# Kernel optimization log

Measured on AMD Instinct MI355X. Metric: run time of the kernel, lower is better.

## Reference

```python
import jax, jax.numpy as jnp
import numpy as np

N = 20000      # num_atoms
C = 64         # num_features (channels)
I = 16         # num_irreps = (l_max+1)^2, l_max=3
K2, K1, K0 = 120, 8, 4  # CG basis sizes per correlation order


def setup_inputs() -> dict:
    key = jax.random.key(0)
    ks = jax.random.split(key, 7)
    return {
        "node_feats": jax.random.normal(ks[0], (N, C, I), jnp.float32),
        "U2": jax.random.normal(ks[1], (I, I, I, K2), jnp.float32),
        "U1": jax.random.normal(ks[2], (I, I, K1), jnp.float32),
        "U0": jax.random.normal(ks[3], (I, K0), jnp.float32),
        "w2": jax.random.normal(ks[4], (K2, C), jnp.float32),
        "w1": jax.random.normal(ks[5], (K1, C), jnp.float32),
        "w0": jax.random.normal(ks[6], (K0, C), jnp.float32),
    }


def reference(node_feats, U2, U1, U0, w2, w1, w0):
    # equation_main: '...ik,kc,bci -> bc...' with U2 [I,I,I,K2]
    # -> out [N, C, I, I]
    out = jnp.einsum('xyik,kc,nci->ncxy', U2, w2, node_feats)

    # corr = 1: weighting '...k,kc->c...' then contract 'bc...i,bci->bc...'
    c1 = jnp.einsum('xik,kc->cxi', U1, w1)          # [C, I, I]
    out = jnp.einsum('ncxi,nci->ncx', c1 + out, node_feats)  # [N, C, I]

    # corr = 0
    c0 = jnp.einsum('ik,kc->ci', U0, w0)            # [C, I]
    out = jnp.einsum('nci,nci->nc', c0 + out, node_feats)    # [N, C]
    return out
```

## Files before the change

kernel.cpp:

```cpp
#include <hip/hip_runtime.h>

#define NATOMS 20000
#define NCHAN  64
#define NIRR   16
#define K2 120
#define K1 8
#define K0 4

#define W1_BYTE_OFF 524288
#define W0_BYTE_OFF 557056

#define NT 10

typedef __attribute__((ext_vector_type(8))) short bf16x8;
typedef __attribute__((ext_vector_type(4))) float f32x4;
typedef __attribute__((ext_vector_type(4))) unsigned int u32x4;

__device__ inline short f2bf(float f) {
    union { float f; unsigned u; } v; v.f = f;
    unsigned r = v.u + 0x7FFF + ((v.u >> 16) & 1);
    return (short)(r >> 16);
}

__global__ __launch_bounds__(256) void precompute_kernel(
    const float* __restrict__ U2, const float* __restrict__ U1,
    const float* __restrict__ U0, const float* __restrict__ w2,
    const float* __restrict__ w1, const float* __restrict__ w0,
    void* __restrict__ wsv)
{
    short* W2bf = (short*)wsv;
    short* W1bf = (short*)((char*)wsv + W1_BYTE_OFF);
    float* W0f  = (float*)((char*)wsv + W0_BYTE_OFF);

    const int b = blockIdx.x;
    const int t = threadIdx.x;

    if (b < 256) {
        __shared__ __align__(16) float U2s[64][121];
        __shared__ __align__(16) float w2s[120][16];
        const int xyi0  = (b >> 2) * 64;
        const int cbase = (b & 3) * 16;

        for (int o = t; o < 64 * 120; o += 256) {
            int r = o / 120, k = o - r * 120;
            U2s[r][k] = U2[(size_t)xyi0 * 120 + o];
        }
        for (int o = t; o < 120 * 16; o += 256) {
            int k = o >> 4, cc = o & 15;
            w2s[k][cc] = w2[k * NCHAN + cbase + cc];
        }
        __syncthreads();

        const int r = t & 63;
        const int g = t >> 6;
        float acc0 = 0.f, acc1 = 0.f, acc2 = 0.f, acc3 = 0.f;
        #pragma unroll 8
        for (int k = 0; k < 120; ++k) {
            float u = U2s[r][k];
            float4 w = *(const float4*)&w2s[k][g * 4];
            acc0 += u * w.x; acc1 += u * w.y; acc2 += u * w.z; acc3 += u * w.w;
        }
        const int xyi = xyi0 + r;
        const int cA  = cbase + g * 4;
        W2bf[(size_t)(cA + 0) * 4096 + xyi] = f2bf(acc0);
        W2bf[(size_t)(cA + 1) * 4096 + xyi] = f2bf(acc1);
        W2bf[(size_t)(cA + 2) * 4096 + xyi] = f2bf(acc2);
        W2bf[(size_t)(cA + 3) * 4096 + xyi] = f2bf(acc3);
    } else {
        const int lb = b - 256;
        for (int o = t; o < 2048; o += 256) {
            int go = lb * 2048 + o;
            int c = go >> 8, xy = go & 255;
            const float* u = U1 + xy * K1;
            float acc = 0.f;
            #pragma unroll
            for (int k = 0; k < K1; ++k) acc += u[k] * w1[k * NCHAN + c];
            W1bf[c * 256 + xy] = f2bf(acc);
        }
        if (lb == 0) {
            for (int o = t; o < 1024; o += 256) {
                int c = o >> 4, x = o & 15;
                const float* u = U0 + x * K0;
                float acc = 0.f;
                #pragma unroll
                for (int k = 0; k < K0; ++k) acc += u[k] * w0[k * NCHAN + c];
                W0f[c * 16 + x] = acc;
            }
        }
    }
}

__device__ __forceinline__ void gload_lds16(const void* g, void* l) {
    __builtin_amdgcn_global_load_lds(
        (const __attribute__((address_space(1))) unsigned int*)g,
        (__attribute__((address_space(3))) unsigned int*)l, 16, 0, 0);
}

__device__ __forceinline__ float compute_tile(
    const bf16x8 (&aw)[16], float4 c0, int q,
    float4 va, float4 vb, float4 vc, float4 vd)
{
    float f0 = va.x, f1 = va.y, f2 = va.z, f3 = va.w;
    float f4 = vb.x, f5 = vb.y, f6 = vb.z, f7 = vb.w;
    float f8 = vc.x, f9 = vc.y, f10 = vc.z, f11 = vc.w;
    float f12 = vd.x, f13 = vd.y, f14 = vd.z, f15 = vd.w;

    unsigned pk0, pk1, pk2, pk3, pk4, pk5, pk6, pk7;
    asm("v_cvt_pk_bf16_f32 %0, %1, %2" : "=v"(pk0) : "v"(f0),  "v"(f1));
    asm("v_cvt_pk_bf16_f32 %0, %1, %2" : "=v"(pk1) : "v"(f2),  "v"(f3));
    asm("v_cvt_pk_bf16_f32 %0, %1, %2" : "=v"(pk2) : "v"(f4),  "v"(f5));
    asm("v_cvt_pk_bf16_f32 %0, %1, %2" : "=v"(pk3) : "v"(f6),  "v"(f7));
    asm("v_cvt_pk_bf16_f32 %0, %1, %2" : "=v"(pk4) : "v"(f8),  "v"(f9));
    asm("v_cvt_pk_bf16_f32 %0, %1, %2" : "=v"(pk5) : "v"(f10), "v"(f11));
    asm("v_cvt_pk_bf16_f32 %0, %1, %2" : "=v"(pk6) : "v"(f12), "v"(f13));
    asm("v_cvt_pk_bf16_f32 %0, %1, %2" : "=v"(pk7) : "v"(f14), "v"(f15));

    unsigned w0s = (q == 0) ? pk0 : (q == 1) ? pk4 : (q == 2) ? 0x00003f80u : 0u;
    unsigned w1s = (q == 0) ? pk1 : (q == 1) ? pk5 : 0u;
    unsigned w2s_ = (q == 0) ? pk2 : (q == 1) ? pk6 : 0u;
    unsigned w3s = (q == 0) ? pk3 : (q == 1) ? pk7 : 0u;
    u32x4 bu = {w0s, w1s, w2s_, w3s};
    bf16x8 bfr = __builtin_bit_cast(bf16x8, bu);

    const f32x4 z = {0.f, 0.f, 0.f, 0.f};
    f32x4 syA = z, syB = z;
    f32x4 d0 = __builtin_amdgcn_mfma_f32_16x16x32_bf16(aw[0], bfr, z, 0, 0, 0);
    f32x4 d1 = __builtin_amdgcn_mfma_f32_16x16x32_bf16(aw[1], bfr, z, 0, 0, 0);
    f32x4 d2 = __builtin_amdgcn_mfma_f32_16x16x32_bf16(aw[2], bfr, z, 0, 0, 0);
    f32x4 d3 = __builtin_amdgcn_mfma_f32_16x16x32_bf16(aw[3], bfr, z, 0, 0, 0);
    syA += d0 * f0;  d0 = __builtin_amdgcn_mfma_f32_16x16x32_bf16(aw[4],  bfr, z, 0, 0, 0);
    syB += d1 * f1;  d1 = __builtin_amdgcn_mfma_f32_16x16x32_bf16(aw[5],  bfr, z, 0, 0, 0);
    syA += d2 * f2;  d2 = __builtin_amdgcn_mfma_f32_16x16x32_bf16(aw[6],  bfr, z, 0, 0, 0);
    syB += d3 * f3;  d3 = __builtin_amdgcn_mfma_f32_16x16x32_bf16(aw[7],  bfr, z, 0, 0, 0);
    syA += d0 * f4;  d0 = __builtin_amdgcn_mfma_f32_16x16x32_bf16(aw[8],  bfr, z, 0, 0, 0);
    syB += d1 * f5;  d1 = __builtin_amdgcn_mfma_f32_16x16x32_bf16(aw[9],  bfr, z, 0, 0, 0);
    syA += d2 * f6;  d2 = __builtin_amdgcn_mfma_f32_16x16x32_bf16(aw[10], bfr, z, 0, 0, 0);
    syB += d3 * f7;  d3 = __builtin_amdgcn_mfma_f32_16x16x32_bf16(aw[11], bfr, z, 0, 0, 0);
    syA += d0 * f8;  d0 = __builtin_amdgcn_mfma_f32_16x16x32_bf16(aw[12], bfr, z, 0, 0, 0);
    syB += d1 * f9;  d1 = __builtin_amdgcn_mfma_f32_16x16x32_bf16(aw[13], bfr, z, 0, 0, 0);
    syA += d2 * f10; d2 = __builtin_amdgcn_mfma_f32_16x16x32_bf16(aw[14], bfr, z, 0, 0, 0);
    syB += d3 * f11; d3 = __builtin_amdgcn_mfma_f32_16x16x32_bf16(aw[15], bfr, z, 0, 0, 0);
    syA += d0 * f12; syB += d1 * f13; syA += d2 * f14; syB += d3 * f15;
    f32x4 sy = syA + syB;

    float t0 = (q & 1) ? f4 : f0;   float u0 = (q & 1) ? f12 : f8;
    float fy0 = (q & 2) ? u0 : t0;
    float t1 = (q & 1) ? f5 : f1;   float u1 = (q & 1) ? f13 : f9;
    float fy1 = (q & 2) ? u1 : t1;
    float t2 = (q & 1) ? f6 : f2;   float u2 = (q & 1) ? f14 : f10;
    float fy2 = (q & 2) ? u2 : t2;
    float t3 = (q & 1) ? f7 : f3;   float u3 = (q & 1) ? f15 : f11;
    float fy3 = (q & 2) ? u3 : t3;

    float s = fy0 * (sy.x + c0.x);
    s = fmaf(fy1, sy.y + c0.y, s);
    s = fmaf(fy2, sy.z + c0.z, s);
    s = fmaf(fy3, sy.w + c0.w, s);
    s += __shfl_xor(s, 16);
    s += __shfl_xor(s, 32);
    return s;
}

__global__ __launch_bounds__(256, 4) void contract_kernel(
    const float* __restrict__ nf,
    const void* __restrict__ wsv,
    float* __restrict__ out)
{
    __shared__ __align__(16) float fs[NT][1024];

    const short* W2g = (const short*)wsv;
    const short* W1g = (const short*)((const char*)wsv + W1_BYTE_OFF);
    const float* W0g = (const float*)((const char*)wsv + W0_BYTE_OFF);

    const int tid  = threadIdx.x;
    const int wave = tid >> 6;
    const int lane = tid & 63;
    const int m    = lane & 15;
    const int q    = lane >> 4;
    const int c    = blockIdx.x * 4 + wave;
    const int chunk = blockIdx.y;

    const int a_st = tid >> 4;
    const int o_l  = (tid & 15) << 4;
    const int o_g  = o_l ^ (a_st << 4);
    const char* sbase = (const char*)nf
        + ((size_t)(chunk * 160 + a_st) << 12)
        + ((size_t)blockIdx.x << 8)
        + o_g;
    const unsigned ldw = (unsigned)(wave << 10);

    #pragma unroll
    for (int t = 0; t < NT; ++t)
        gload_lds16(sbase + (size_t)t * 65536, (char*)&fs[t][0] + ldw);

    bf16x8 aw[16];
    #pragma unroll
    for (int j = 0; j < 16; ++j) {
        bf16x8 v = (bf16x8)0;
        if (q < 2) {
            v = *(const bf16x8*)(W2g + ((size_t)c << 12) + ((j * 16 + m) << 4) + (q << 3));
        } else if (q == 2) {
            v[0] = W1g[(c << 8) + (j << 4) + m];
        }
        aw[j] = v;
    }
    const float4 c0 = *(const float4*)(W0g + (c << 4) + (q << 2));

    asm volatile("s_waitcnt vmcnt(0)" ::: "memory");
    __builtin_amdgcn_s_barrier();
    __builtin_amdgcn_sched_barrier(0);

    const unsigned sw = (unsigned)(m << 4);
    const unsigned zb = (unsigned)(wave << 6);

    float outv[NT];

    #pragma unroll
    for (int T = 0; T < NT; ++T) {
        const char* lrb = (const char*)&fs[T][0] + (m << 8);
        float4 va = *(const float4*)(lrb + ((zb +  0) ^ sw));
        float4 vb = *(const float4*)(lrb + ((zb + 16) ^ sw));
        float4 vc = *(const float4*)(lrb + ((zb + 32) ^ sw));
        float4 vd = *(const float4*)(lrb + ((zb + 48) ^ sw));
        outv[T] = compute_tile(aw, c0, q, va, vb, vc, vd);
    }

    if (q == 0) {
        float* ob = out + ((size_t)(chunk * 160 + m)) * 64 + c;
        #pragma unroll
        for (int T = 0; T < NT; ++T)
            ob[(size_t)T * 1024] = outv[T];
    }
}

extern "C" void kernel_launch(void* const* d_in, const int* in_sizes, int n_in,
                              void* d_out, int out_size, void* d_ws, size_t ws_size,
                              hipStream_t stream)
{
    const float* nf = (const float*)d_in[0];
    const float* U2 = (const float*)d_in[1];
    const float* U1 = (const float*)d_in[2];
    const float* U0 = (const float*)d_in[3];
    const float* w2 = (const float*)d_in[4];
    const float* w1 = (const float*)d_in[5];
    const float* w0 = (const float*)d_in[6];
    float* out = (float*)d_out;

    precompute_kernel<<<264, 256, 0, stream>>>(U2, U1, U0, w2, w1, w0, d_ws);

    dim3 grid(16, 125);
    contract_kernel<<<grid, 256, 0, stream>>>(nf, d_ws, out);
}
```

Baseline: 164.4 us.

## Give each wave private LDS tiles and pipeline loads with per-tile waits

Each of 8 waves per block now stages only its own channel's node features into a private LDS region, so the block-wide barrier is gone. Feature loads are issued after the weight loads, and each tile waits only for its own data through a decreasing vmcnt count, overlapping memory with compute. Blocks grow to 512 threads and each handles 80 atoms instead of 160, which changes the grid shape. The launch bound of (512,4) may force a much tighter register budget and cause spills of the 16-entry weight fragment.

```diff
diff --git a/kernel.cpp b/kernel.cpp
--- a/kernel.cpp
+++ b/kernel.cpp
@@ -10,7 +10,7 @@
 #define W1_BYTE_OFF 524288
 #define W0_BYTE_OFF 557056
 
-#define NT 10
+#define NT 5
 
 typedef __attribute__((ext_vector_type(8))) short bf16x8;
 typedef __attribute__((ext_vector_type(4))) float f32x4;
@@ -161,12 +161,12 @@
     return s;
 }
 
-__global__ __launch_bounds__(256, 4) void contract_kernel(
+__global__ __launch_bounds__(512, 4) void contract_kernel(
     const float* __restrict__ nf,
     const void* __restrict__ wsv,
     float* __restrict__ out)
 {
-    __shared__ __align__(16) float fs[NT][1024];
+    __shared__ __align__(16) char fs[8][NT][1024];
 
     const short* W2g = (const short*)wsv;
     const short* W1g = (const short*)((const char*)wsv + W1_BYTE_OFF);
@@ -177,21 +177,17 @@
     const int lane = tid & 63;
     const int m    = lane & 15;
     const int q    = lane >> 4;
-    const int c    = blockIdx.x * 4 + wave;
-    const int chunk = blockIdx.y;
-
-    const int a_st = tid >> 4;
-    const int o_l  = (tid & 15) << 4;
-    const int o_g  = o_l ^ (a_st << 4);
+    const int c    = blockIdx.x * 8 + wave;
+    const int atom0 = blockIdx.y * 80;
+
+    const int a_st = lane >> 2;
+    const int r_st = lane & 3;
+    const int srcj = (r_st - (a_st >> 2)) & 3;
     const char* sbase = (const char*)nf
-        + ((size_t)(chunk * 160 + a_st) << 12)
-        + ((size_t)blockIdx.x << 8)
-        + o_g;
-    const unsigned ldw = (unsigned)(wave << 10);
-
-    #pragma unroll
-    for (int t = 0; t < NT; ++t)
-        gload_lds16(sbase + (size_t)t * 65536, (char*)&fs[t][0] + ldw);
+        + ((size_t)(atom0 + a_st) << 12)
+        + (c << 6)
+        + (srcj << 4);
+    char* ldst = &fs[wave][0][0];
 
     bf16x8 aw[16];
     #pragma unroll
@@ -207,26 +203,35 @@
     const float4 c0 = *(const float4*)(W0g + (c << 4) + (q << 2));
 
     asm volatile("s_waitcnt vmcnt(0)" ::: "memory");
-    __builtin_amdgcn_s_barrier();
     __builtin_amdgcn_sched_barrier(0);
 
-    const unsigned sw = (unsigned)(m << 4);
-    const unsigned zb = (unsigned)(wave << 6);
+    #pragma unroll
+    for (int t = 0; t < NT; ++t)
+        gload_lds16(sbase + (size_t)t * 65536, ldst + t * 1024);
+    __builtin_amdgcn_sched_barrier(0);
 
     float outv[NT];
 
     #pragma unroll
     for (int T = 0; T < NT; ++T) {
-        const char* lrb = (const char*)&fs[T][0] + (m << 8);
-        float4 va = *(const float4*)(lrb + ((zb +  0) ^ sw));
-        float4 vb = *(const float4*)(lrb + ((zb + 16) ^ sw));
-        float4 vc = *(const float4*)(lrb + ((zb + 32) ^ sw));
-        float4 vd = *(const float4*)(lrb + ((zb + 48) ^ sw));
+        if      (T == 0) asm volatile("s_waitcnt vmcnt(4)" ::: "memory");
+        else if (T == 1) asm volatile("s_waitcnt vmcnt(3)" ::: "memory");
+        else if (T == 2) asm volatile("s_waitcnt vmcnt(2)" ::: "memory");
+        else if (T == 3) asm volatile("s_waitcnt vmcnt(1)" ::: "memory");
+        else             asm volatile("s_waitcnt vmcnt(0)" ::: "memory");
+        __builtin_amdgcn_sched_barrier(0);
+
+        const char* lrb = &fs[wave][T][0] + (m << 6);
+        float4 va = *(const float4*)(lrb + ((((0 + (m >> 2)) & 3)) << 4));
+        float4 vb = *(const float4*)(lrb + ((((1 + (m >> 2)) & 3)) << 4));
+        float4 vc = *(const float4*)(lrb + ((((2 + (m >> 2)) & 3)) << 4));
+        float4 vd = *(const float4*)(lrb + ((((3 + (m >> 2)) & 3)) << 4));
+
         outv[T] = compute_tile(aw, c0, q, va, vb, vc, vd);
     }
 
     if (q == 0) {
-        float* ob = out + ((size_t)(chunk * 160 + m)) * 64 + c;
+        float* ob = out + ((size_t)(atom0 + m)) * 64 + c;
         #pragma unroll
         for (int T = 0; T < NT; ++T)
             ob[(size_t)T * 1024] = outv[T];
@@ -248,6 +253,6 @@
 
     precompute_kernel<<<264, 256, 0, stream>>>(U2, U1, U0, w2, w1, w0, d_ws);
 
-    dim3 grid(16, 125);
-    contract_kernel<<<grid, 256, 0, stream>>>(nf, d_ws, out);
-}
+    dim3 grid(8, 250);
+    contract_kernel<<<grid, 512, 0, stream>>>(nf, d_ws, out);
+}
```

New measurement: 162.0 us. About the same (-1.4%).
